# Kernel tuning notes

Hardware: AMD Instinct MI355X
Metric: run time of the kernel (lower is better)

The kernel has to match this reference:

```python
import jax, jax.numpy as jnp
import numpy as np

E, S, Q, NN_NODES, R = 2048, 256, 25, 36, 15
H = 128  # MLP hidden width


def setup_inputs() -> dict:
    key = jax.random.key(0)
    ks = jax.random.split(key, 16)
    g = lambda k, shape, scale=1.0: (jax.random.normal(k, shape, dtype=jnp.float32) * scale)
    inp = {
        "nodes": g(ks[0], (E, NN_NODES, 2)),
        "W1": g(ks[1], (2, H), 1.0 / np.sqrt(2.0)),
        "b1": jnp.zeros((H,), jnp.float32),
        "W2": g(ks[2], (H, H), 1.0 / np.sqrt(H)),
        "b2": jnp.zeros((H,), jnp.float32),
        "W3": g(ks[3], (H, H), 1.0 / np.sqrt(H)),
        "b3": jnp.zeros((H,), jnp.float32),
        "W4": g(ks[4], (H, 1), 1.0 / np.sqrt(H)),
        "b4": jnp.zeros((1,), jnp.float32),
        # 2nd-derivative interpolation matrices of the inter basis B at the
        # sub-element quadrature points (shared across big elements).
        "Ixx": g(ks[5], (S, Q, NN_NODES), 0.1),
        "Iyy": g(ks[6], (S, Q, NN_NODES), 0.1),
        # per-big-element 2x2 Hessian change-of-coordinates map (B_DD_inter)
        "B_DD": g(ks[7], (E, 2, 2)),
        "w_quad": jax.random.uniform(ks[8], (Q,), dtype=jnp.float32),
        # test-function values at quadrature points (b.Base)
        "Base": g(ks[9], (Q, R)),
        # per-sub-element Jacobians and precomputed RHS projections F_total
        "J": jax.random.uniform(ks[10], (E, S), dtype=jnp.float32),
        "F": g(ks[11], (E, S, R)),
    }
    return inp


def _mlp(x, W1, b1, W2, b2, W3, b3, W4, b4):
    h = jnp.tanh(x @ W1 + b1)
    h = jnp.tanh(h @ W2 + b2)
    h = jnp.tanh(h @ W3 + b3)
    return h @ W4 + b4


def reference(nodes, W1, b1, W2, b2, W3, b3, W4, b4,
              Ixx, Iyy, B_DD, w_quad, Base, J, F):
    # NN evaluated once per big element at its interpolation nodes: [E, n_nodes]
    ev = _mlp(nodes.reshape(-1, 2), W1, b1, W2, b2, W3, b3, W4, b4)
    ev = ev.reshape(E, NN_NODES)
    d2x = jnp.einsum("sqn,en->esq", Ixx, ev)
    d2y = jnp.einsum("sqn,en->esq", Iyy, ev)
    grad_second = jnp.stack([d2x, d2y], axis=2)           # [E,S,2,Q]
    # B_DD_inter @ grad_second^T, per big element
    grad_second = jnp.einsum("eij,esjq->esiq", B_DD, grad_second)
    integrand_1 = grad_second.sum(axis=2)                 # [E,S,Q]
    # u_NN_el[r] = -J * sum_q w[q] * Base[q,r] * integrand_1[q]
    u_el = -J[:, :, None] * jnp.einsum("q,qr,esq->esr", w_quad, Base, integrand_1)
    res = u_el - F                                        # [E,S,R]
    # loss_element = mean over test functions, summed over all (big, sub) elements
    return jnp.sum(jnp.mean(jnp.square(res), axis=-1))
```

## Files before the change

### kernel.cpp

```cpp
#include <hip/hip_runtime.h>

#define EN 2048
#define SN 256
#define QN 25
#define NNODES 36
#define RN 15
#define HN 128
#define KP 96
#define NTOT (SN * RN)

typedef __attribute__((ext_vector_type(8))) short short8;
typedef __attribute__((ext_vector_type(4))) float f32x4;
typedef __attribute__((ext_vector_type(2))) unsigned int uint2v;

__device__ __forceinline__ unsigned short f2bf(float f) {
    unsigned int u = __float_as_uint(f);
    u += 0x7fffu + ((u >> 16) & 1u);
    return (unsigned short)(u >> 16);
}
__device__ __forceinline__ float bf2f(unsigned short h) {
    return __uint_as_float(((unsigned int)h) << 16);
}
__device__ __forceinline__ float fast_tanh(float x) {
    float e = __builtin_amdgcn_exp2f(x * 2.885390082f);
    float r = __builtin_amdgcn_rcpf(e + 1.f);
    return fmaf(-2.f, r, 1.f);
}

__device__ __forceinline__ void load_W(const float* __restrict__ W,
                                       unsigned short (*Ws)[136], int t)
{
    const int n = t & 127;
    const int h = t >> 7;
    #pragma unroll
    for (int kk = 0; kk < 16; kk++) {
        const int k0 = (kk * 2 + h) * 4;
        const float a0 = W[(k0 + 0) * HN + n];
        const float a1 = W[(k0 + 1) * HN + n];
        const float a2 = W[(k0 + 2) * HN + n];
        const float a3 = W[(k0 + 3) * HN + n];
        uint2v pk;
        pk[0] = (unsigned)f2bf(a0) | ((unsigned)f2bf(a1) << 16);
        pk[1] = (unsigned)f2bf(a2) | ((unsigned)f2bf(a3) << 16);
        *(uint2v*)&Ws[n][k0] = pk;
    }
}

__device__ __forceinline__ void mfma_layer(unsigned short (*Hs)[136],
                                           const unsigned short (*Ws)[136],
                                           const float* __restrict__ bias,
                                           int wv, int rowA, int quad)
{
    const int r0 = wv * 32;
    short8 afrag[2][4];
    #pragma unroll
    for (int rt = 0; rt < 2; rt++)
        #pragma unroll
        for (int kt = 0; kt < 4; kt++)
            afrag[rt][kt] = *(const short8*)&Hs[r0 + rt * 16 + rowA][kt * 32 + quad * 8];

    f32x4 acc[2][8];
    const f32x4 zero = {0.f, 0.f, 0.f, 0.f};
    #pragma unroll
    for (int rt = 0; rt < 2; rt++)
        #pragma unroll
        for (int nt = 0; nt < 8; nt++) acc[rt][nt] = zero;

    #pragma unroll
    for (int nt = 0; nt < 8; nt++) {
        #pragma unroll
        for (int kt = 0; kt < 4; kt++) {
            const short8 bfrag = *(const short8*)&Ws[nt * 16 + rowA][kt * 32 + quad * 8];
            acc[0][nt] = __builtin_amdgcn_mfma_f32_16x16x32_bf16(afrag[0][kt], bfrag, acc[0][nt], 0, 0, 0);
            acc[1][nt] = __builtin_amdgcn_mfma_f32_16x16x32_bf16(afrag[1][kt], bfrag, acc[1][nt], 0, 0, 0);
        }
    }
    #pragma unroll
    for (int nt = 0; nt < 8; nt++) {
        const int col = nt * 16 + rowA;
        const float bv = bias[col];
        #pragma unroll
        for (int rt = 0; rt < 2; rt++) {
            #pragma unroll
            for (int rg = 0; rg < 4; rg++) {
                const float v = fast_tanh(acc[rt][nt][rg] + bv);
                Hs[r0 + rt * 16 + quad * 4 + rg][col] = f2bf(v);
            }
        }
    }
}

#define MC_BLOCKS  SN
#define MLP_BLOCKS 576

__global__ __launch_bounds__(256, 2)
void prep_kernel(const float* __restrict__ nodes,
                 const float* __restrict__ W1, const float* __restrict__ b1,
                 const float* __restrict__ W2, const float* __restrict__ b2,
                 const float* __restrict__ W3, const float* __restrict__ b3,
                 const float* __restrict__ W4, const float* __restrict__ b4,
                 const float* __restrict__ B_DD,
                 const float* __restrict__ Ixx, const float* __restrict__ Iyy,
                 const float* __restrict__ wq, const float* __restrict__ Base,
                 const float* __restrict__ Fin, const float* __restrict__ Jin,
                 unsigned short* __restrict__ evcb,
                 unsigned short* __restrict__ Mcb,
                 float* __restrict__ out)
{
    __shared__ unsigned short Hs[128][136];
    __shared__ unsigned short Ws[128][136];
    __shared__ float WB[QN * 16];
    const int bid = blockIdx.x;
    const int t   = threadIdx.x;

    if (bid >= MC_BLOCKS) {
        const int mb   = bid - MC_BLOCKS;
        const int lane = t & 63;
        const int wv   = t >> 6;
        const int rowA = lane & 15;
        const int quad = lane >> 4;

        {
            const int p  = t >> 1;
            const int P  = mb * 128 + p;
            const float x0 = nodes[2 * P], x1 = nodes[2 * P + 1];
            const int n0 = (t & 1) * 64;
            #pragma unroll
            for (int i = 0; i < 16; i++) {
                const int n = n0 + 4 * i;
                const float4 wa = *(const float4*)(W1 + n);
                const float4 wb = *(const float4*)(W1 + HN + n);
                const float4 bb = *(const float4*)(b1 + n);
                const float h0 = fast_tanh(fmaf(x0, wa.x, fmaf(x1, wb.x, bb.x)));
                const float h1 = fast_tanh(fmaf(x0, wa.y, fmaf(x1, wb.y, bb.y)));
                const float h2 = fast_tanh(fmaf(x0, wa.z, fmaf(x1, wb.z, bb.z)));
                const float h3 = fast_tanh(fmaf(x0, wa.w, fmaf(x1, wb.w, bb.w)));
                uint2v pk;
                pk[0] = (unsigned)f2bf(h0) | ((unsigned)f2bf(h1) << 16);
                pk[1] = (unsigned)f2bf(h2) | ((unsigned)f2bf(h3) << 16);
                *(uint2v*)&Hs[p][n] = pk;
            }
        }
        load_W(W2, Ws, t);
        __syncthreads();
        mfma_layer(Hs, Ws, b2, wv, rowA, quad);
        __syncthreads();
        load_W(W3, Ws, t);
        __syncthreads();
        mfma_layer(Hs, Ws, b3, wv, rowA, quad);
        {
            const int p  = t >> 1;
            const int k0 = (t & 1) * 64;
            float d = 0.f;
            #pragma unroll
            for (int i = 0; i < 8; i++) {
                const short8 h = *(const short8*)&Hs[p][k0 + 8 * i];
                const float4 wA = *(const float4*)(W4 + k0 + 8 * i);
                const float4 wB = *(const float4*)(W4 + k0 + 8 * i + 4);
                d = fmaf(bf2f((unsigned short)h[0]), wA.x, d);
                d = fmaf(bf2f((unsigned short)h[1]), wA.y, d);
                d = fmaf(bf2f((unsigned short)h[2]), wA.z, d);
                d = fmaf(bf2f((unsigned short)h[3]), wA.w, d);
                d = fmaf(bf2f((unsigned short)h[4]), wB.x, d);
                d = fmaf(bf2f((unsigned short)h[5]), wB.y, d);
                d = fmaf(bf2f((unsigned short)h[6]), wB.z, d);
                d = fmaf(bf2f((unsigned short)h[7]), wB.w, d);
            }
            d += __shfl_xor(d, 1, 64);
            if ((t & 1) == 0) {
                const float ev = d + b4[0];
                const int P  = mb * 128 + p;
                const int e  = P / NNODES;
                const int ne = P - e * NNODES;
                const float c0 = B_DD[4 * e + 0] + B_DD[4 * e + 2];
                const float c1 = B_DD[4 * e + 1] + B_DD[4 * e + 3];
                evcb[e * KP + ne]          = f2bf(c0 * ev);
                evcb[e * KP + NNODES + ne] = f2bf(c1 * ev);
                if (ne < KP - 2 * NNODES)
                    evcb[e * KP + 2 * NNODES + ne] = 0;
            }
        }
    } else {
        const int s = bid;
        if (s == 0 && t == 0) out[0] = 0.f;
        float* I_lds = (float*)&Hs[0][0];
        for (int i = t; i < QN * 16; i += 256) {
            const int q = i >> 4, r = i & 15;
            if (r < RN) WB[i] = wq[q] * Base[q * RN + r];
        }
        const float* __restrict__ Ia = Ixx + (size_t)s * (QN * NNODES);
        const float* __restrict__ Ib = Iyy + (size_t)s * (QN * NNODES);
        for (int i = t; i < QN * NNODES; i += 256) {
            I_lds[i]               = Ia[i];
            I_lds[QN * NNODES + i] = Ib[i];
        }
        __syncthreads();
        for (int o = t; o < RN * KP; o += 256) {
            const int c = o % KP;
            const int r = o / KP;
            float v = 0.f;
            if (c < 2 * NNODES) {
                const float* __restrict__ Ip =
                    I_lds + ((c < NNODES) ? c : (QN * NNODES + c - NNODES));
                float a0 = 0.f, a1 = 0.f;
                #pragma unroll
                for (int q = 0; q < QN - 1; q += 2) {
                    a0 = fmaf(WB[q * 16 + r],       Ip[q * NNODES],       a0);
                    a1 = fmaf(WB[(q + 1) * 16 + r], Ip[(q + 1) * NNODES], a1);
                }
                a0 = fmaf(WB[(QN - 1) * 16 + r], Ip[(QN - 1) * NNODES], a0);
                v = a0 + a1;
            }
            Mcb[((size_t)s * RN + r) * KP + c] = f2bf(v);
        }
        {
            const size_t base = (size_t)s * 256 + t;
            const size_t stride = (size_t)MC_BLOCKS * 256;
            const float4* F4 = (const float4*)Fin;
            const size_t nF4 = (size_t)EN * NTOT / 4;
            for (size_t i = base; i < nF4; i += stride) {
                float4 v = F4[i];
                asm volatile("" :: "v"(v.x), "v"(v.y), "v"(v.z), "v"(v.w));
            }
            const float4* J4 = (const float4*)Jin;
            const size_t nJ4 = (size_t)EN * SN / 4;
            for (size_t i = base; i < nJ4; i += stride) {
                float4 v = J4[i];
                asm volatile("" :: "v"(v.x), "v"(v.y), "v"(v.z), "v"(v.w));
            }
        }
    }
}

__global__ __launch_bounds__(256, 4)
void loss_kernel(const unsigned short* __restrict__ evcb,
                 const unsigned short* __restrict__ Mcb,
                 const float* __restrict__ J, const float* __restrict__ F,
                 float* __restrict__ out)
{
    const int t    = threadIdx.x;
    const int lane = t & 63;
    const int wv   = t >> 6;
    const int rowA = lane & 15;
    const int quad = lane >> 4;
    const int m0 = (blockIdx.x & 31) * 64;
    const int n0 = (blockIdx.x >> 5) * 128 + wv * 32;

    float Fv[2][16];
    #pragma unroll
    for (int nt = 0; nt < 2; nt++) {
        const int n = n0 + nt * 16 + rowA;
        #pragma unroll
        for (int mt = 0; mt < 4; mt++)
            #pragma unroll
            for (int rg = 0; rg < 4; rg++)
                Fv[nt][mt * 4 + rg] = F[(size_t)(m0 + mt * 16 + quad * 4 + rg) * NTOT + n];
    }

    f32x4 acc[4][2];
    const f32x4 zero = {0.f, 0.f, 0.f, 0.f};
    #pragma unroll
    for (int mt = 0; mt < 4; mt++)
        #pragma unroll
        for (int nt = 0; nt < 2; nt++) acc[mt][nt] = zero;

    #pragma unroll
    for (int kt = 0; kt < 3; kt++) {
        short8 a[4], b[2];
        #pragma unroll
        for (int mt = 0; mt < 4; mt++)
            a[mt] = *(const short8*)&evcb[(size_t)(m0 + mt * 16 + rowA) * KP + kt * 32 + quad * 8];
        #pragma unroll
        for (int nt = 0; nt < 2; nt++)
            b[nt] = *(const short8*)&Mcb[(size_t)(n0 + nt * 16 + rowA) * KP + kt * 32 + quad * 8];
        #pragma unroll
        for (int mt = 0; mt < 4; mt++)
            #pragma unroll
            for (int nt = 0; nt < 2; nt++)
                acc[mt][nt] = __builtin_amdgcn_mfma_f32_16x16x32_bf16(a[mt], b[nt], acc[mt][nt], 0, 0, 0);
    }

    float total = 0.f;
    #pragma unroll
    for (int nt = 0; nt < 2; nt++) {
        const int n = n0 + nt * 16 + rowA;
        const int s = (n * 34953) >> 19;
        #pragma unroll
        for (int mt = 0; mt < 4; mt++) {
            const int eb = m0 + mt * 16 + quad * 4;
            #pragma unroll
            for (int rg = 0; rg < 4; rg++) {
                const float Jv = J[(size_t)(eb + rg) * SN + s];
                const float d  = acc[mt][nt][rg];
                const float res = fmaf(-Jv, d, -Fv[nt][mt * 4 + rg]);
                total = fmaf(res, res, total);
            }
        }
    }
    total *= (1.f / (float)RN);

    #pragma unroll
    for (int off = 32; off; off >>= 1)
        total += __shfl_down(total, off, 64);
    __shared__ float wsum[4];
    if (lane == 0) wsum[wv] = total;
    __syncthreads();
    if (t == 0) atomicAdd(out, (wsum[0] + wsum[1]) + (wsum[2] + wsum[3]));
}

extern "C" void kernel_launch(void* const* d_in, const int* in_sizes, int n_in,
                              void* d_out, int out_size, void* d_ws, size_t ws_size,
                              hipStream_t stream)
{
    (void)in_sizes; (void)n_in; (void)out_size; (void)ws_size;
    const float* nodes = (const float*)d_in[0];
    const float* W1   = (const float*)d_in[1];
    const float* b1   = (const float*)d_in[2];
    const float* W2   = (const float*)d_in[3];
    const float* b2   = (const float*)d_in[4];
    const float* W3   = (const float*)d_in[5];
    const float* b3   = (const float*)d_in[6];
    const float* W4   = (const float*)d_in[7];
    const float* b4   = (const float*)d_in[8];
    const float* Ixx  = (const float*)d_in[9];
    const float* Iyy  = (const float*)d_in[10];
    const float* B_DD = (const float*)d_in[11];
    const float* wq   = (const float*)d_in[12];
    const float* Base = (const float*)d_in[13];
    const float* J    = (const float*)d_in[14];
    const float* F    = (const float*)d_in[15];
    float* out = (float*)d_out;
    unsigned short* evcb = (unsigned short*)d_ws;
    unsigned short* Mcb  = (unsigned short*)((char*)d_ws + EN * KP * 2);

    prep_kernel<<<MC_BLOCKS + MLP_BLOCKS, 256, 0, stream>>>(
        nodes, W1, b1, W2, b2, W3, b3, W4, b4, B_DD, Ixx, Iyy, wq, Base,
        F, J, evcb, Mcb, out);
    loss_kernel<<<32 * 30, 256, 0, stream>>>(evcb, Mcb, J, F, out);
}
```

Measured before the change: 146.4 us.

## Split MLP weight staging into halves and drop F/J cache prefetch

Each hidden MLP layer now stages its weight matrix into shared memory in two 64-column halves instead of all at once. This halves the Ws footprint and the accumulator register count, so the occupancy bound rises from 2 to 3 blocks. The cost is extra __syncthreads per layer. The MC blocks also stop doing dummy reads of F and J that warmed the cache for the loss kernel, which may make the loss kernel pay full memory latency on those inputs.

```diff
diff --git a/kernel.cpp b/kernel.cpp
--- a/kernel.cpp
+++ b/kernel.cpp
@@ -27,57 +27,51 @@
     return fmaf(-2.f, r, 1.f);
 }
 
-__device__ __forceinline__ void load_W(const float* __restrict__ W,
-                                       unsigned short (*Ws)[136], int t)
-{
-    const int n = t & 127;
-    const int h = t >> 7;
-    #pragma unroll
-    for (int kk = 0; kk < 16; kk++) {
-        const int k0 = (kk * 2 + h) * 4;
-        const float a0 = W[(k0 + 0) * HN + n];
-        const float a1 = W[(k0 + 1) * HN + n];
-        const float a2 = W[(k0 + 2) * HN + n];
-        const float a3 = W[(k0 + 3) * HN + n];
+__device__ __forceinline__ void load_Wh(const float* __restrict__ W,
+                                        unsigned short (*Wh)[136], int t, int half)
+{
+    const int n = t & 63;
+    const int q = t >> 6;
+    const int col = half * 64 + n;
+    #pragma unroll
+    for (int i = 0; i < 8; i++) {
+        const int k0 = q * 32 + i * 4;
+        const float a0 = W[(k0 + 0) * HN + col];
+        const float a1 = W[(k0 + 1) * HN + col];
+        const float a2 = W[(k0 + 2) * HN + col];
+        const float a3 = W[(k0 + 3) * HN + col];
         uint2v pk;
         pk[0] = (unsigned)f2bf(a0) | ((unsigned)f2bf(a1) << 16);
         pk[1] = (unsigned)f2bf(a2) | ((unsigned)f2bf(a3) << 16);
-        *(uint2v*)&Ws[n][k0] = pk;
-    }
-}
-
-__device__ __forceinline__ void mfma_layer(unsigned short (*Hs)[136],
-                                           const unsigned short (*Ws)[136],
-                                           const float* __restrict__ bias,
-                                           int wv, int rowA, int quad)
-{
-    const int r0 = wv * 32;
-    short8 afrag[2][4];
+        *(uint2v*)&Wh[n][k0] = pk;
+    }
+}
+
+__device__ __forceinline__ void mfma_half(unsigned short (*Hs)[136],
+                                          const unsigned short (*Wh)[136],
+                                          const float* __restrict__ bias,
+                                          const short8 afrag[2][4],
+                                          int r0, int rowA, int quad, int half)
+{
+    f32x4 acc[2][4];
+    const f32x4 zero = {0.f, 0.f, 0.f, 0.f};
     #pragma unroll
     for (int rt = 0; rt < 2; rt++)
         #pragma unroll
-        for (int kt = 0; kt < 4; kt++)
-            afrag[rt][kt] = *(const short8*)&Hs[r0 + rt * 16 + rowA][kt * 32 + quad * 8];
-
-    f32x4 acc[2][8];
-    const f32x4 zero = {0.f, 0.f, 0.f, 0.f};
-    #pragma unroll
-    for (int rt = 0; rt < 2; rt++)
-        #pragma unroll
-        for (int nt = 0; nt < 8; nt++) acc[rt][nt] = zero;
-
-    #pragma unroll
-    for (int nt = 0; nt < 8; nt++) {
+        for (int nt = 0; nt < 4; nt++) acc[rt][nt] = zero;
+
+    #pragma unroll
+    for (int nt = 0; nt < 4; nt++) {
         #pragma unroll
         for (int kt = 0; kt < 4; kt++) {
-            const short8 bfrag = *(const short8*)&Ws[nt * 16 + rowA][kt * 32 + quad * 8];
+            const short8 bfrag = *(const short8*)&Wh[nt * 16 + rowA][kt * 32 + quad * 8];
             acc[0][nt] = __builtin_amdgcn_mfma_f32_16x16x32_bf16(afrag[0][kt], bfrag, acc[0][nt], 0, 0, 0);
             acc[1][nt] = __builtin_amdgcn_mfma_f32_16x16x32_bf16(afrag[1][kt], bfrag, acc[1][nt], 0, 0, 0);
         }
     }
     #pragma unroll
-    for (int nt = 0; nt < 8; nt++) {
-        const int col = nt * 16 + rowA;
+    for (int nt = 0; nt < 4; nt++) {
+        const int col = half * 64 + nt * 16 + rowA;
         const float bv = bias[col];
         #pragma unroll
         for (int rt = 0; rt < 2; rt++) {
@@ -93,7 +87,7 @@
 #define MC_BLOCKS  SN
 #define MLP_BLOCKS 576
 
-__global__ __launch_bounds__(256, 2)
+__global__ __launch_bounds__(256, 3)
 void prep_kernel(const float* __restrict__ nodes,
                  const float* __restrict__ W1, const float* __restrict__ b1,
                  const float* __restrict__ W2, const float* __restrict__ b2,
@@ -102,13 +96,12 @@
                  const float* __restrict__ B_DD,
                  const float* __restrict__ Ixx, const float* __restrict__ Iyy,
                  const float* __restrict__ wq, const float* __restrict__ Base,
-                 const float* __restrict__ Fin, const float* __restrict__ Jin,
                  unsigned short* __restrict__ evcb,
                  unsigned short* __restrict__ Mcb,
                  float* __restrict__ out)
 {
     __shared__ unsigned short Hs[128][136];
-    __shared__ unsigned short Ws[128][136];
+    __shared__ unsigned short Ws[64][136];
     __shared__ float WB[QN * 16];
     const int bid = blockIdx.x;
     const int t   = threadIdx.x;
@@ -119,6 +112,7 @@
         const int wv   = t >> 6;
         const int rowA = lane & 15;
         const int quad = lane >> 4;
+        const int r0   = wv * 32;
 
         {
             const int p  = t >> 1;
@@ -141,13 +135,36 @@
                 *(uint2v*)&Hs[p][n] = pk;
             }
         }
-        load_W(W2, Ws, t);
-        __syncthreads();
-        mfma_layer(Hs, Ws, b2, wv, rowA, quad);
-        __syncthreads();
-        load_W(W3, Ws, t);
-        __syncthreads();
-        mfma_layer(Hs, Ws, b3, wv, rowA, quad);
+        short8 afrag[2][4];
+        {
+            load_Wh(W2, Ws, t, 0);
+            #pragma unroll
+            for (int rt = 0; rt < 2; rt++)
+                #pragma unroll
+                for (int kt = 0; kt < 4; kt++)
+                    afrag[rt][kt] = *(const short8*)&Hs[r0 + rt * 16 + rowA][kt * 32 + quad * 8];
+            __syncthreads();
+            mfma_half(Hs, Ws, b2, afrag, r0, rowA, quad, 0);
+            __syncthreads();
+            load_Wh(W2, Ws, t, 1);
+            __syncthreads();
+            mfma_half(Hs, Ws, b2, afrag, r0, rowA, quad, 1);
+            __syncthreads();
+        }
+        {
+            load_Wh(W3, Ws, t, 0);
+            #pragma unroll
+            for (int rt = 0; rt < 2; rt++)
+                #pragma unroll
+                for (int kt = 0; kt < 4; kt++)
+                    afrag[rt][kt] = *(const short8*)&Hs[r0 + rt * 16 + rowA][kt * 32 + quad * 8];
+            __syncthreads();
+            mfma_half(Hs, Ws, b3, afrag, r0, rowA, quad, 0);
+            __syncthreads();
+            load_Wh(W3, Ws, t, 1);
+            __syncthreads();
+            mfma_half(Hs, Ws, b3, afrag, r0, rowA, quad, 1);
+        }
         {
             const int p  = t >> 1;
             const int k0 = (t & 1) * 64;
@@ -212,22 +229,6 @@
                 v = a0 + a1;
             }
             Mcb[((size_t)s * RN + r) * KP + c] = f2bf(v);
-        }
-        {
-            const size_t base = (size_t)s * 256 + t;
-            const size_t stride = (size_t)MC_BLOCKS * 256;
-            const float4* F4 = (const float4*)Fin;
-            const size_t nF4 = (size_t)EN * NTOT / 4;
-            for (size_t i = base; i < nF4; i += stride) {
-                float4 v = F4[i];
-                asm volatile("" :: "v"(v.x), "v"(v.y), "v"(v.z), "v"(v.w));
-            }
-            const float4* J4 = (const float4*)Jin;
-            const size_t nJ4 = (size_t)EN * SN / 4;
-            for (size_t i = base; i < nJ4; i += stride) {
-                float4 v = J4[i];
-                asm volatile("" :: "v"(v.x), "v"(v.y), "v"(v.z), "v"(v.w));
-            }
         }
     }
 }
@@ -335,6 +336,6 @@
 
     prep_kernel<<<MC_BLOCKS + MLP_BLOCKS, 256, 0, stream>>>(
         nodes, W1, b1, W2, b2, W3, b3, W4, b4, B_DD, Ixx, Iyy, wq, Base,
-        F, J, evcb, Mcb, out);
+        evcb, Mcb, out);
     loss_kernel<<<32 * 30, 256, 0, stream>>>(evcb, Mcb, J, F, out);
 }
```

Measured after the change: 144.1 us. No clear change (-1.6%).
